# Optimization experiments

Measured on AMD Instinct MI355X. Metric: run time of the kernel, lower is better.

The kernel has to match this reference:

```python
import jax, jax.numpy as jnp
import numpy as np


def setup_inputs() -> dict:
    key = jax.random.key(0)
    kq, kk, kv = jax.random.split(key, 3)
    B, N, D = 8, 4096, 128
    Q = jax.random.normal(kq, (B, N, D), dtype=jnp.float32)
    K = jax.random.normal(kk, (B, N, D), dtype=jnp.float32)
    V = jax.random.normal(kv, (B, N, D), dtype=jnp.float32)
    return {"Q": Q, "K": K, "V": V}


def reference(Q, K, V):
    # attention = Q @ K^T  -> [B, N, N]  (scale=None, mask=None path)
    attention = jnp.einsum('bnd,bmd->bnm', Q, K)
    attention = jax.nn.softmax(attention, axis=-1)
    # context = attention @ V -> [B, N, D]
    context = jnp.einsum('bnm,bmd->bnd', attention, V)
    return context
```

## Files before the change

kernel.cpp:

```cpp
#include <hip/hip_runtime.h>

#define NB 8
#define SEQ 4096
#define DIM 128
#define KVB 64
#define NTILES (SEQ / KVB)
#define HALF 32
#define IMG_BYTES 32768
#define IMG_TOTAL ((size_t)NB * NTILES * IMG_BYTES)
#define PART_ELEMS ((size_t)NB * SEQ * DIM)
#define PART_BYTES (PART_ELEMS * 4)
#define LS_ELEMS ((size_t)NB * SEQ)
#define WS_SPLIT (IMG_TOTAL + 2 * PART_BYTES + 2 * LS_ELEMS * 4)
#define WS_BASIC IMG_TOTAL
#define L2E 1.44269504088896f

typedef _Float16 f16x8 __attribute__((ext_vector_type(8)));
typedef __bf16 bf16x8 __attribute__((ext_vector_type(8)));
typedef float f32x4 __attribute__((ext_vector_type(4)));
typedef float f32x16 __attribute__((ext_vector_type(16)));

struct U4 { unsigned x, y, z, w; };

static __device__ __forceinline__ unsigned cvtpk_bf16(float a, float b) {
  unsigned d;
  asm("v_cvt_pk_bf16_f32 %0, %1, %2" : "=v"(d) : "v"(a), "v"(b));
  return d;
}

#define EXP2(x) __builtin_amdgcn_exp2f(x)

__global__ void prep_kv(const float* __restrict__ K, const float* __restrict__ V,
                        unsigned char* __restrict__ ws) {
  const int t = blockIdx.x;
  const int b = blockIdx.y;
  unsigned char* img = ws + ((size_t)b * NTILES + t) * IMG_BYTES;
  int4* kimg = (int4*)img;
  int4* vimg = (int4*)(img + 16384);
  const float* Kb = K + ((size_t)b * SEQ + t * KVB) * DIM;
  const float* Vb = V + ((size_t)b * SEQ + t * KVB) * DIM;
  const int tid = threadIdx.x;

#pragma unroll
  for (int p = 0; p < 4; ++p) {
    const int un = tid + 256 * p;
    const int kv = un >> 4;
    const int u = (un & 15) ^ (kv & 15);
    const int s = u >> 1, hh = u & 1;
    const float* src = Kb + (size_t)kv * DIM + 16 * s + 8 * hh;
    f16x8 hv;
#pragma unroll
    for (int j = 0; j < 8; ++j) hv[j] = (_Float16)src[j];
    kimg[un] = __builtin_bit_cast(int4, hv);
  }

#pragma unroll
  for (int p = 0; p < 4; ++p) {
    const int un = tid + 256 * p;
    const int rr = un >> 4;
    const int c = (un & 15) ^ (rr & 15);
    const int dhi = c >> 3, slot = c & 7;
    const int s2 = slot >> 1, hh = slot & 1;
    const int d = 64 * dhi + rr;
    bf16x8 hv;
#pragma unroll
    for (int e = 0; e < 8; ++e) {
      const int kv = 16 * s2 + 4 * hh + (e & 3) + 8 * (e >> 2);
      hv[e] = (__bf16)Vb[(size_t)kv * DIM + d];
    }
    vimg[un] = __builtin_bit_cast(int4, hv);
  }
}

__global__ __launch_bounds__(256, 1)
void attn_split(const float* __restrict__ Q, const unsigned char* __restrict__ ws,
                float* __restrict__ part, float* __restrict__ lsw) {
  __shared__ __align__(16) unsigned char smem[65536];

  const int tid = threadIdx.x;
  const int w4 = tid >> 6;
  const int l = tid & 63;
  const int l31 = l & 31;
  const int h = l >> 5;

  const int bid = blockIdx.x;
  const int b = bid & 7;
  const int kvh = (bid >> 3) & 1;
  const int qt = bid >> 4;
  const size_t base = (size_t)b * SEQ * DIM;
  const int qrow0 = qt * 256 + w4 * 64 + l31;

  f16x8 qfA[8], qfB[8];
#pragma unroll
  for (int qb = 0; qb < 2; ++qb) {
    const float* qp = Q + base + (size_t)(qrow0 + 32 * qb) * DIM + 8 * h;
#pragma unroll
    for (int s = 0; s < 8; ++s) {
      f32x4 a = *(const f32x4*)(qp + 16 * s);
      f32x4 c = *(const f32x4*)(qp + 16 * s + 4);
      f16x8 hv;
#pragma unroll
      for (int j = 0; j < 4; ++j) {
        hv[j] = (_Float16)(a[j] * L2E);
        hv[j + 4] = (_Float16)(c[j] * L2E);
      }
      if (qb == 0) qfA[s] = hv; else qfB[s] = hv;
    }
  }

  f32x16 oA[4], oB[4];
#pragma unroll
  for (int j = 0; j < 4; ++j) {
#pragma unroll
    for (int r = 0; r < 16; ++r) { oA[j][r] = 0.f; oB[j][r] = 0.f; }
  }
  float lsA = 0.f, lsB = 0.f;

  const unsigned char* wsb = ws + (size_t)b * NTILES * IMG_BYTES;

  auto STAGE = [&](int t, int bufsel) {
    const unsigned char* src = wsb + (size_t)t * IMG_BYTES + w4 * 8192 + l * 16;
    unsigned char* dst = smem + bufsel * 32768 + w4 * 8192;
#pragma unroll
    for (int i = 0; i < 8; ++i) {
      __builtin_amdgcn_global_load_lds(
          (const __attribute__((address_space(1))) unsigned int*)(src + i * 1024),
          (__attribute__((address_space(3))) unsigned int*)(dst + i * 1024),
          16, 0, 0);
    }
  };

  const int kb2 = (l31 * 256 + ((l31 & 15) * 16)) ^ (h * 16);
  int vb[4];
#pragma unroll
  for (int j = 0; j < 4; ++j) {
    const int rr = 32 * (j & 1) + l31;
    vb[j] = 16384 + rr * 256 + ((((j >> 1) * 8 + h) ^ (rr & 15)) * 16);
  }

  const int t0 = kvh * HALF;
  STAGE(t0, 0);
  __syncthreads();

#pragma unroll 1
  for (int i = 0; i < HALF; ++i) {
    const int cur = i & 1;
    if (i + 1 < HALF) STAGE(t0 + i + 1, cur ^ 1);
    const unsigned char* bufp = smem + cur * 32768;

    f16x8 kk0[8], kk1[8];
#pragma unroll
    for (int s = 0; s < 8; ++s) {
      kk0[s] = *(const f16x8*)(bufp + (kb2 ^ (32 * s)));
      kk1[s] = *(const f16x8*)(bufp + (kb2 ^ (32 * s)) + 8192);
    }

    f32x16 s0, s1, r0, r1;
#pragma unroll
    for (int r = 0; r < 16; ++r) { s0[r] = 0.f; s1[r] = 0.f; r0[r] = 0.f; r1[r] = 0.f; }
    __builtin_amdgcn_s_setprio(1);
#pragma unroll
    for (int s = 0; s < 8; ++s) {
      s0 = __builtin_amdgcn_mfma_f32_32x32x16_f16(kk0[s], qfA[s], s0, 0, 0, 0);
      s1 = __builtin_amdgcn_mfma_f32_32x32x16_f16(kk1[s], qfA[s], s1, 0, 0, 0);
    }
#pragma unroll
    for (int s = 0; s < 8; ++s) {
      r0 = __builtin_amdgcn_mfma_f32_32x32x16_f16(kk0[s], qfB[s], r0, 0, 0, 0);
      r1 = __builtin_amdgcn_mfma_f32_32x32x16_f16(kk1[s], qfB[s], r1, 0, 0, 0);
    }
    __builtin_amdgcn_s_setprio(0);

    bf16x8 vf[16];
#pragma unroll
    for (int s2 = 0; s2 < 4; ++s2) {
#pragma unroll
      for (int j = 0; j < 4; ++j)
        vf[4 * s2 + j] = *(const bf16x8*)(bufp + (vb[j] ^ (32 * s2)));
    }

    float a0 = 0.f, a1 = 0.f, a2 = 0.f, a3 = 0.f;
#pragma unroll
    for (int r = 0; r < 16; r += 4) {
      s0[r + 0] = EXP2(s0[r + 0]); s0[r + 1] = EXP2(s0[r + 1]);
      s0[r + 2] = EXP2(s0[r + 2]); s0[r + 3] = EXP2(s0[r + 3]);
      a0 += s0[r + 0]; a1 += s0[r + 1]; a2 += s0[r + 2]; a3 += s0[r + 3];
    }
#pragma unroll
    for (int r = 0; r < 16; r += 4) {
      s1[r + 0] = EXP2(s1[r + 0]); s1[r + 1] = EXP2(s1[r + 1]);
      s1[r + 2] = EXP2(s1[r + 2]); s1[r + 3] = EXP2(s1[r + 3]);
      a0 += s1[r + 0]; a1 += s1[r + 1]; a2 += s1[r + 2]; a3 += s1[r + 3];
    }
    lsA += (a0 + a1) + (a2 + a3);
    bf16x8 pbA[4];
#pragma unroll
    for (int u = 0; u < 2; ++u) {
      U4 ta = {cvtpk_bf16(s0[8 * u + 0], s0[8 * u + 1]),
               cvtpk_bf16(s0[8 * u + 2], s0[8 * u + 3]),
               cvtpk_bf16(s0[8 * u + 4], s0[8 * u + 5]),
               cvtpk_bf16(s0[8 * u + 6], s0[8 * u + 7])};
      U4 tb = {cvtpk_bf16(s1[8 * u + 0], s1[8 * u + 1]),
               cvtpk_bf16(s1[8 * u + 2], s1[8 * u + 3]),
               cvtpk_bf16(s1[8 * u + 4], s1[8 * u + 5]),
               cvtpk_bf16(s1[8 * u + 6], s1[8 * u + 7])};
      pbA[u] = __builtin_bit_cast(bf16x8, ta);
      pbA[2 + u] = __builtin_bit_cast(bf16x8, tb);
    }

    __builtin_amdgcn_s_setprio(1);
#pragma unroll
    for (int s2 = 0; s2 < 4; ++s2) {
#pragma unroll
      for (int j = 0; j < 4; ++j)
        oA[j] = __builtin_amdgcn_mfma_f32_32x32x16_bf16(vf[4 * s2 + j], pbA[s2],
                                                        oA[j], 0, 0, 0);
    }
    __builtin_amdgcn_s_setprio(0);

    float b0 = 0.f, b1 = 0.f, b2 = 0.f, b3 = 0.f;
#pragma unroll
    for (int r = 0; r < 16; r += 4) {
      r0[r + 0] = EXP2(r0[r + 0]); r0[r + 1] = EXP2(r0[r + 1]);
      r0[r + 2] = EXP2(r0[r + 2]); r0[r + 3] = EXP2(r0[r + 3]);
      b0 += r0[r + 0]; b1 += r0[r + 1]; b2 += r0[r + 2]; b3 += r0[r + 3];
    }
#pragma unroll
    for (int r = 0; r < 16; r += 4) {
      r1[r + 0] = EXP2(r1[r + 0]); r1[r + 1] = EXP2(r1[r + 1]);
      r1[r + 2] = EXP2(r1[r + 2]); r1[r + 3] = EXP2(r1[r + 3]);
      b0 += r1[r + 0]; b1 += r1[r + 1]; b2 += r1[r + 2]; b3 += r1[r + 3];
    }
    lsB += (b0 + b1) + (b2 + b3);
    bf16x8 pbB[4];
#pragma unroll
    for (int u = 0; u < 2; ++u) {
      U4 ta = {cvtpk_bf16(r0[8 * u + 0], r0[8 * u + 1]),
               cvtpk_bf16(r0[8 * u + 2], r0[8 * u + 3]),
               cvtpk_bf16(r0[8 * u + 4], r0[8 * u + 5]),
               cvtpk_bf16(r0[8 * u + 6], r0[8 * u + 7])};
      U4 tb = {cvtpk_bf16(r1[8 * u + 0], r1[8 * u + 1]),
               cvtpk_bf16(r1[8 * u + 2], r1[8 * u + 3]),
               cvtpk_bf16(r1[8 * u + 4], r1[8 * u + 5]),
               cvtpk_bf16(r1[8 * u + 6], r1[8 * u + 7])};
      pbB[u] = __builtin_bit_cast(bf16x8, ta);
      pbB[2 + u] = __builtin_bit_cast(bf16x8, tb);
    }

    __builtin_amdgcn_s_setprio(1);
#pragma unroll
    for (int s2 = 0; s2 < 4; ++s2) {
#pragma unroll
      for (int j = 0; j < 4; ++j)
        oB[j] = __builtin_amdgcn_mfma_f32_32x32x16_bf16(vf[4 * s2 + j], pbB[s2],
                                                        oB[j], 0, 0, 0);
    }
    __builtin_amdgcn_s_setprio(0);
    __syncthreads();
  }

  lsA += __shfl_xor(lsA, 32);
  lsB += __shfl_xor(lsB, 32);
  float* P = part + (size_t)kvh * PART_ELEMS + base;
#pragma unroll
  for (int qb = 0; qb < 2; ++qb) {
    float* Pb = P + (size_t)(qrow0 + 32 * qb) * DIM;
#pragma unroll
    for (int j = 0; j < 4; ++j) {
#pragma unroll
      for (int rq = 0; rq < 4; ++rq) {
        f32x4 res;
#pragma unroll
        for (int r = 0; r < 4; ++r)
          res[r] = qb == 0 ? oA[j][4 * rq + r] : oB[j][4 * rq + r];
        *(f32x4*)(Pb + 32 * j + 8 * rq + 4 * h) = res;
      }
    }
  }
  if (h == 0) {
    lsw[(size_t)kvh * LS_ELEMS + b * SEQ + qrow0] = lsA;
    lsw[(size_t)kvh * LS_ELEMS + b * SEQ + qrow0 + 32] = lsB;
  }
}

__global__ void combine(const float* __restrict__ part,
                        const float* __restrict__ lsw,
                        float* __restrict__ out) {
  const size_t idx = (size_t)blockIdx.x * 256 + threadIdx.x;
  const f32x4 a = ((const f32x4*)part)[idx];
  const f32x4 b = ((const f32x4*)(part + PART_ELEMS))[idx];
  const size_t row = idx >> 5;
  const float inv = 1.0f / (lsw[row] + lsw[LS_ELEMS + row]);
  f32x4 r;
#pragma unroll
  for (int j = 0; j < 4; ++j) r[j] = (a[j] + b[j]) * inv;
  ((f32x4*)out)[idx] = r;
}

__global__ __launch_bounds__(256, 2)
void attn_fwd15(const float* __restrict__ Q, const unsigned char* __restrict__ ws,
                float* __restrict__ O) {
  __shared__ __align__(16) unsigned char smem[65536];

  const int tid = threadIdx.x;
  const int w4 = tid >> 6;
  const int l = tid & 63;
  const int l31 = l & 31;
  const int h = l >> 5;

  const int bid = blockIdx.x;
  const int b = bid & 7;
  const int qt = bid >> 3;
  const size_t base = (size_t)b * SEQ * DIM;
  const int qrow = qt * 128 + w4 * 32 + l31;

  f16x8 qf[8];
  {
    const float* qp = Q + base + (size_t)qrow * DIM + 8 * h;
#pragma unroll
    for (int s = 0; s < 8; ++s) {
      f32x4 a = *(const f32x4*)(qp + 16 * s);
      f32x4 c = *(const f32x4*)(qp + 16 * s + 4);
      f16x8 hv;
#pragma unroll
      for (int j = 0; j < 4; ++j) {
        hv[j] = (_Float16)(a[j] * L2E);
        hv[j + 4] = (_Float16)(c[j] * L2E);
      }
      qf[s] = hv;
    }
  }

  f32x16 o[4];
#pragma unroll
  for (int j = 0; j < 4; ++j) {
#pragma unroll
    for (int r = 0; r < 16; ++r) o[j][r] = 0.f;
  }
  float ls = 0.f;

  const unsigned char* wsb = ws + (size_t)b * NTILES * IMG_BYTES;

  auto STAGE = [&](int t, int bufsel) {
    const unsigned char* src = wsb + (size_t)t * IMG_BYTES + w4 * 8192 + l * 16;
    unsigned char* dst = smem + bufsel * 32768 + w4 * 8192;
#pragma unroll
    for (int i = 0; i < 8; ++i) {
      __builtin_amdgcn_global_load_lds(
          (const __attribute__((address_space(1))) unsigned int*)(src + i * 1024),
          (__attribute__((address_space(3))) unsigned int*)(dst + i * 1024),
          16, 0, 0);
    }
  };

  const int kb2 = (l31 * 256 + ((l31 & 15) * 16)) ^ (h * 16);
  int vb[4];
#pragma unroll
  for (int j = 0; j < 4; ++j) {
    const int rr = 32 * (j & 1) + l31;
    vb[j] = 16384 + rr * 256 + ((((j >> 1) * 8 + h) ^ (rr & 15)) * 16);
  }

  STAGE(0, 0);
  __syncthreads();

  for (int t = 0; t < NTILES; ++t) {
    const int cur = t & 1;
    if (t + 1 < NTILES) STAGE(t + 1, cur ^ 1);
    const unsigned char* bufp = smem + cur * 32768;

    f32x16 s0, s1;
#pragma unroll
    for (int r = 0; r < 16; ++r) { s0[r] = 0.f; s1[r] = 0.f; }
    __builtin_amdgcn_s_setprio(1);
#pragma unroll
    for (int s = 0; s < 8; ++s) {
      f16x8 k0 = *(const f16x8*)(bufp + (kb2 ^ (32 * s)));
      s0 = __builtin_amdgcn_mfma_f32_32x32x16_f16(k0, qf[s], s0, 0, 0, 0);
    }
#pragma unroll
    for (int s = 0; s < 8; ++s) {
      f16x8 k1 = *(const f16x8*)(bufp + (kb2 ^ (32 * s)) + 8192);
      s1 = __builtin_amdgcn_mfma_f32_32x32x16_f16(k1, qf[s], s1, 0, 0, 0);
    }
    __builtin_amdgcn_s_setprio(0);

    float a0 = 0.f, a1 = 0.f, a2 = 0.f, a3 = 0.f;
#pragma unroll
    for (int r = 0; r < 16; r += 4) {
      s0[r + 0] = EXP2(s0[r + 0]); s0[r + 1] = EXP2(s0[r + 1]);
      s0[r + 2] = EXP2(s0[r + 2]); s0[r + 3] = EXP2(s0[r + 3]);
      a0 += s0[r + 0]; a1 += s0[r + 1]; a2 += s0[r + 2]; a3 += s0[r + 3];
    }
    bf16x8 pb0[2];
#pragma unroll
    for (int u = 0; u < 2; ++u) {
      U4 t0 = {cvtpk_bf16(s0[8 * u + 0], s0[8 * u + 1]),
               cvtpk_bf16(s0[8 * u + 2], s0[8 * u + 3]),
               cvtpk_bf16(s0[8 * u + 4], s0[8 * u + 5]),
               cvtpk_bf16(s0[8 * u + 6], s0[8 * u + 7])};
      pb0[u] = __builtin_bit_cast(bf16x8, t0);
    }

    __builtin_amdgcn_s_setprio(1);
#pragma unroll
    for (int s2 = 0; s2 < 2; ++s2) {
#pragma unroll
      for (int j = 0; j < 4; ++j) {
        bf16x8 vf = *(const bf16x8*)(bufp + (vb[j] ^ (32 * s2)));
        o[j] = __builtin_amdgcn_mfma_f32_32x32x16_bf16(vf, pb0[s2], o[j], 0, 0, 0);
      }
    }
    __builtin_amdgcn_s_setprio(0);

#pragma unroll
    for (int r = 0; r < 16; r += 4) {
      s1[r + 0] = EXP2(s1[r + 0]); s1[r + 1] = EXP2(s1[r + 1]);
      s1[r + 2] = EXP2(s1[r + 2]); s1[r + 3] = EXP2(s1[r + 3]);
      a0 += s1[r + 0]; a1 += s1[r + 1]; a2 += s1[r + 2]; a3 += s1[r + 3];
    }
    ls += (a0 + a1) + (a2 + a3);
    bf16x8 pb1[2];
#pragma unroll
    for (int u = 0; u < 2; ++u) {
      U4 t1 = {cvtpk_bf16(s1[8 * u + 0], s1[8 * u + 1]),
               cvtpk_bf16(s1[8 * u + 2], s1[8 * u + 3]),
               cvtpk_bf16(s1[8 * u + 4], s1[8 * u + 5]),
               cvtpk_bf16(s1[8 * u + 6], s1[8 * u + 7])};
      pb1[u] = __builtin_bit_cast(bf16x8, t1);
    }

    __builtin_amdgcn_s_setprio(1);
#pragma unroll
    for (int s2 = 2; s2 < 4; ++s2) {
#pragma unroll
      for (int j = 0; j < 4; ++j) {
        bf16x8 vf = *(const bf16x8*)(bufp + (vb[j] ^ (32 * s2)));
        o[j] = __builtin_amdgcn_mfma_f32_32x32x16_bf16(vf, pb1[s2 - 2], o[j], 0, 0, 0);
      }
    }
    __builtin_amdgcn_s_setprio(0);
    __syncthreads();
  }

  ls += __shfl_xor(ls, 32);
  const float inv = 1.0f / ls;
  float* Ob = O + base + (size_t)qrow * DIM;
#pragma unroll
  for (int j = 0; j < 4; ++j) {
#pragma unroll
    for (int rq = 0; rq < 4; ++rq) {
      f32x4 res;
#pragma unroll
      for (int r = 0; r < 4; ++r) res[r] = o[j][4 * rq + r] * inv;
      *(f32x4*)(Ob + 32 * j + 8 * rq + 4 * h) = res;
    }
  }
}

extern "C" void kernel_launch(void* const* d_in, const int* in_sizes, int n_in,
                              void* d_out, int out_size, void* d_ws,
                              size_t ws_size, hipStream_t stream) {
  const float* Q = (const float*)d_in[0];
  const float* K = (const float*)d_in[1];
  const float* V = (const float*)d_in[2];
  float* Out = (float*)d_out;
  unsigned char* ws = (unsigned char*)d_ws;
  if (ws_size < WS_BASIC) return;
  prep_kv<<<dim3(NTILES, NB), dim3(256), 0, stream>>>(K, V, ws);
  if (ws_size >= WS_SPLIT) {
    float* part = (float*)(ws + IMG_TOTAL);
    float* lsw = (float*)(ws + IMG_TOTAL + 2 * PART_BYTES);
    attn_split<<<dim3(256), dim3(256), 0, stream>>>(Q, ws, part, lsw);
    combine<<<dim3(PART_ELEMS / 4 / 256), dim3(256), 0, stream>>>(part, lsw, Out);
  } else {
    attn_fwd15<<<dim3(SEQ / 128 * NB), dim3(256), 0, stream>>>(Q, ws, Out);
  }
}
```

Baseline: 103.3 us.

## Halve per-wave query rows in split kernel to run two blocks per CU

Each wave of the split-KV attention kernel now handles 32 query rows instead of 64. The grid doubles to 512 blocks and launch bounds allow 2 blocks per CU. K and V fragments are loaded from LDS just before each MFMA instead of being preloaded into registers, and the PV product for the first half-tile is interleaved before the second exp pass. The aim is lower register pressure and more resident waves to hide latency, at the cost of reading K/V from LDS twice as often per query row. The 64KB shared buffer per block may limit how many blocks actually fit per CU.

```diff
diff --git a/kernel.cpp b/kernel.cpp
--- a/kernel.cpp
+++ b/kernel.cpp
@@ -72,7 +72,7 @@
   }
 }
 
-__global__ __launch_bounds__(256, 1)
+__global__ __launch_bounds__(256, 2)
 void attn_split(const float* __restrict__ Q, const unsigned char* __restrict__ ws,
                 float* __restrict__ part, float* __restrict__ lsw) {
   __shared__ __align__(16) unsigned char smem[65536];
@@ -88,12 +88,11 @@
   const int kvh = (bid >> 3) & 1;
   const int qt = bid >> 4;
   const size_t base = (size_t)b * SEQ * DIM;
-  const int qrow0 = qt * 256 + w4 * 64 + l31;
-
-  f16x8 qfA[8], qfB[8];
-#pragma unroll
-  for (int qb = 0; qb < 2; ++qb) {
-    const float* qp = Q + base + (size_t)(qrow0 + 32 * qb) * DIM + 8 * h;
+  const int qrow = qt * 128 + w4 * 32 + l31;
+
+  f16x8 qf[8];
+  {
+    const float* qp = Q + base + (size_t)qrow * DIM + 8 * h;
 #pragma unroll
     for (int s = 0; s < 8; ++s) {
       f32x4 a = *(const f32x4*)(qp + 16 * s);
@@ -104,17 +103,17 @@
         hv[j] = (_Float16)(a[j] * L2E);
         hv[j + 4] = (_Float16)(c[j] * L2E);
       }
-      if (qb == 0) qfA[s] = hv; else qfB[s] = hv;
-    }
-  }
-
-  f32x16 oA[4], oB[4];
-#pragma unroll
-  for (int j = 0; j < 4; ++j) {
-#pragma unroll
-    for (int r = 0; r < 16; ++r) { oA[j][r] = 0.f; oB[j][r] = 0.f; }
-  }
-  float lsA = 0.f, lsB = 0.f;
+      qf[s] = hv;
+    }
+  }
+
+  f32x16 o[4];
+#pragma unroll
+  for (int j = 0; j < 4; ++j) {
+#pragma unroll
+    for (int r = 0; r < 16; ++r) o[j][r] = 0.f;
+  }
+  float ls = 0.f;
 
   const unsigned char* wsb = ws + (size_t)b * NTILES * IMG_BYTES;
 
@@ -148,36 +147,21 @@
     if (i + 1 < HALF) STAGE(t0 + i + 1, cur ^ 1);
     const unsigned char* bufp = smem + cur * 32768;
 
-    f16x8 kk0[8], kk1[8];
-#pragma unroll
-    for (int s = 0; s < 8; ++s) {
-      kk0[s] = *(const f16x8*)(bufp + (kb2 ^ (32 * s)));
-      kk1[s] = *(const f16x8*)(bufp + (kb2 ^ (32 * s)) + 8192);
-    }
-
-    f32x16 s0, s1, r0, r1;
-#pragma unroll
-    for (int r = 0; r < 16; ++r) { s0[r] = 0.f; s1[r] = 0.f; r0[r] = 0.f; r1[r] = 0.f; }
-    __builtin_amdgcn_s_setprio(1);
-#pragma unroll
-    for (int s = 0; s < 8; ++s) {
-      s0 = __builtin_amdgcn_mfma_f32_32x32x16_f16(kk0[s], qfA[s], s0, 0, 0, 0);
-      s1 = __builtin_amdgcn_mfma_f32_32x32x16_f16(kk1[s], qfA[s], s1, 0, 0, 0);
-    }
-#pragma unroll
-    for (int s = 0; s < 8; ++s) {
-      r0 = __builtin_amdgcn_mfma_f32_32x32x16_f16(kk0[s], qfB[s], r0, 0, 0, 0);
-      r1 = __builtin_amdgcn_mfma_f32_32x32x16_f16(kk1[s], qfB[s], r1, 0, 0, 0);
-    }
-    __builtin_amdgcn_s_setprio(0);
-
-    bf16x8 vf[16];
-#pragma unroll
-    for (int s2 = 0; s2 < 4; ++s2) {
-#pragma unroll
-      for (int j = 0; j < 4; ++j)
-        vf[4 * s2 + j] = *(const bf16x8*)(bufp + (vb[j] ^ (32 * s2)));
-    }
+    f32x16 s0, s1;
+#pragma unroll
+    for (int r = 0; r < 16; ++r) { s0[r] = 0.f; s1[r] = 0.f; }
+    __builtin_amdgcn_s_setprio(1);
+#pragma unroll
+    for (int s = 0; s < 8; ++s) {
+      f16x8 k0 = *(const f16x8*)(bufp + (kb2 ^ (32 * s)));
+      s0 = __builtin_amdgcn_mfma_f32_32x32x16_f16(k0, qf[s], s0, 0, 0, 0);
+    }
+#pragma unroll
+    for (int s = 0; s < 8; ++s) {
+      f16x8 k1 = *(const f16x8*)(bufp + (kb2 ^ (32 * s)) + 8192);
+      s1 = __builtin_amdgcn_mfma_f32_32x32x16_f16(k1, qf[s], s1, 0, 0, 0);
+    }
+    __builtin_amdgcn_s_setprio(0);
 
     float a0 = 0.f, a1 = 0.f, a2 = 0.f, a3 = 0.f;
 #pragma unroll
@@ -186,101 +170,70 @@
       s0[r + 2] = EXP2(s0[r + 2]); s0[r + 3] = EXP2(s0[r + 3]);
       a0 += s0[r + 0]; a1 += s0[r + 1]; a2 += s0[r + 2]; a3 += s0[r + 3];
     }
+    bf16x8 pb0[2];
+#pragma unroll
+    for (int u = 0; u < 2; ++u) {
+      U4 t0v = {cvtpk_bf16(s0[8 * u + 0], s0[8 * u + 1]),
+                cvtpk_bf16(s0[8 * u + 2], s0[8 * u + 3]),
+                cvtpk_bf16(s0[8 * u + 4], s0[8 * u + 5]),
+                cvtpk_bf16(s0[8 * u + 6], s0[8 * u + 7])};
+      pb0[u] = __builtin_bit_cast(bf16x8, t0v);
+    }
+
+    __builtin_amdgcn_s_setprio(1);
+#pragma unroll
+    for (int s2 = 0; s2 < 2; ++s2) {
+#pragma unroll
+      for (int j = 0; j < 4; ++j) {
+        bf16x8 vf = *(const bf16x8*)(bufp + (vb[j] ^ (32 * s2)));
+        o[j] = __builtin_amdgcn_mfma_f32_32x32x16_bf16(vf, pb0[s2], o[j], 0, 0, 0);
+      }
+    }
+    __builtin_amdgcn_s_setprio(0);
+
 #pragma unroll
     for (int r = 0; r < 16; r += 4) {
       s1[r + 0] = EXP2(s1[r + 0]); s1[r + 1] = EXP2(s1[r + 1]);
       s1[r + 2] = EXP2(s1[r + 2]); s1[r + 3] = EXP2(s1[r + 3]);
       a0 += s1[r + 0]; a1 += s1[r + 1]; a2 += s1[r + 2]; a3 += s1[r + 3];
     }
-    lsA += (a0 + a1) + (a2 + a3);
-    bf16x8 pbA[4];
+    ls += (a0 + a1) + (a2 + a3);
+    bf16x8 pb1[2];
 #pragma unroll
     for (int u = 0; u < 2; ++u) {
-      U4 ta = {cvtpk_bf16(s0[8 * u + 0], s0[8 * u + 1]),
-               cvtpk_bf16(s0[8 * u + 2], s0[8 * u + 3]),
-               cvtpk_bf16(s0[8 * u + 4], s0[8 * u + 5]),
-               cvtpk_bf16(s0[8 * u + 6], s0[8 * u + 7])};
-      U4 tb = {cvtpk_bf16(s1[8 * u + 0], s1[8 * u + 1]),
-               cvtpk_bf16(s1[8 * u + 2], s1[8 * u + 3]),
-               cvtpk_bf16(s1[8 * u + 4], s1[8 * u + 5]),
-               cvtpk_bf16(s1[8 * u + 6], s1[8 * u + 7])};
-      pbA[u] = __builtin_bit_cast(bf16x8, ta);
-      pbA[2 + u] = __builtin_bit_cast(bf16x8, tb);
-    }
-
-    __builtin_amdgcn_s_setprio(1);
-#pragma unroll
-    for (int s2 = 0; s2 < 4; ++s2) {
-#pragma unroll
-      for (int j = 0; j < 4; ++j)
-        oA[j] = __builtin_amdgcn_mfma_f32_32x32x16_bf16(vf[4 * s2 + j], pbA[s2],
-                                                        oA[j], 0, 0, 0);
-    }
-    __builtin_amdgcn_s_setprio(0);
-
-    float b0 = 0.f, b1 = 0.f, b2 = 0.f, b3 = 0.f;
-#pragma unroll
-    for (int r = 0; r < 16; r += 4) {
-      r0[r + 0] = EXP2(r0[r + 0]); r0[r + 1] = EXP2(r0[r + 1]);
-      r0[r + 2] = EXP2(r0[r + 2]); r0[r + 3] = EXP2(r0[r + 3]);
-      b0 += r0[r + 0]; b1 += r0[r + 1]; b2 += r0[r + 2]; b3 += r0[r + 3];
-    }
-#pragma unroll
-    for (int r = 0; r < 16; r += 4) {
-      r1[r + 0] = EXP2(r1[r + 0]); r1[r + 1] = EXP2(r1[r + 1]);
-      r1[r + 2] = EXP2(r1[r + 2]); r1[r + 3] = EXP2(r1[r + 3]);
-      b0 += r1[r + 0]; b1 += r1[r + 1]; b2 += r1[r + 2]; b3 += r1[r + 3];
-    }
-    lsB += (b0 + b1) + (b2 + b3);
-    bf16x8 pbB[4];
-#pragma unroll
-    for (int u = 0; u < 2; ++u) {
-      U4 ta = {cvtpk_bf16(r0[8 * u + 0], r0[8 * u + 1]),
-               cvtpk_bf16(r0[8 * u + 2], r0[8 * u + 3]),
-               cvtpk_bf16(r0[8 * u + 4], r0[8 * u + 5]),
-               cvtpk_bf16(r0[8 * u + 6], r0[8 * u + 7])};
-      U4 tb = {cvtpk_bf16(r1[8 * u + 0], r1[8 * u + 1]),
-               cvtpk_bf16(r1[8 * u + 2], r1[8 * u + 3]),
-               cvtpk_bf16(r1[8 * u + 4], r1[8 * u + 5]),
-               cvtpk_bf16(r1[8 * u + 6], r1[8 * u + 7])};
-      pbB[u] = __builtin_bit_cast(bf16x8, ta);
-      pbB[2 + u] = __builtin_bit_cast(bf16x8, tb);
-    }
-
-    __builtin_amdgcn_s_setprio(1);
-#pragma unroll
-    for (int s2 = 0; s2 < 4; ++s2) {
-#pragma unroll
-      for (int j = 0; j < 4; ++j)
-        oB[j] = __builtin_amdgcn_mfma_f32_32x32x16_bf16(vf[4 * s2 + j], pbB[s2],
-                                                        oB[j], 0, 0, 0);
+      U4 t1v = {cvtpk_bf16(s1[8 * u + 0], s1[8 * u + 1]),
+                cvtpk_bf16(s1[8 * u + 2], s1[8 * u + 3]),
+                cvtpk_bf16(s1[8 * u + 4], s1[8 * u + 5]),
+                cvtpk_bf16(s1[8 * u + 6], s1[8 * u + 7])};
+      pb1[u] = __builtin_bit_cast(bf16x8, t1v);
+    }
+
+    __builtin_amdgcn_s_setprio(1);
+#pragma unroll
+    for (int s2 = 2; s2 < 4; ++s2) {
+#pragma unroll
+      for (int j = 0; j < 4; ++j) {
+        bf16x8 vf = *(const bf16x8*)(bufp + (vb[j] ^ (32 * s2)));
+        o[j] = __builtin_amdgcn_mfma_f32_32x32x16_bf16(vf, pb1[s2 - 2], o[j], 0, 0, 0);
+      }
     }
     __builtin_amdgcn_s_setprio(0);
     __syncthreads();
   }
 
-  lsA += __shfl_xor(lsA, 32);
-  lsB += __shfl_xor(lsB, 32);
-  float* P = part + (size_t)kvh * PART_ELEMS + base;
-#pragma unroll
-  for (int qb = 0; qb < 2; ++qb) {
-    float* Pb = P + (size_t)(qrow0 + 32 * qb) * DIM;
-#pragma unroll
-    for (int j = 0; j < 4; ++j) {
-#pragma unroll
-      for (int rq = 0; rq < 4; ++rq) {
-        f32x4 res;
-#pragma unroll
-        for (int r = 0; r < 4; ++r)
-          res[r] = qb == 0 ? oA[j][4 * rq + r] : oB[j][4 * rq + r];
-        *(f32x4*)(Pb + 32 * j + 8 * rq + 4 * h) = res;
-      }
-    }
-  }
-  if (h == 0) {
-    lsw[(size_t)kvh * LS_ELEMS + b * SEQ + qrow0] = lsA;
-    lsw[(size_t)kvh * LS_ELEMS + b * SEQ + qrow0 + 32] = lsB;
-  }
+  ls += __shfl_xor(ls, 32);
+  float* Pb = part + (size_t)kvh * PART_ELEMS + base + (size_t)qrow * DIM;
+#pragma unroll
+  for (int j = 0; j < 4; ++j) {
+#pragma unroll
+    for (int rq = 0; rq < 4; ++rq) {
+      f32x4 res;
+#pragma unroll
+      for (int r = 0; r < 4; ++r) res[r] = o[j][4 * rq + r];
+      *(f32x4*)(Pb + 32 * j + 8 * rq + 4 * h) = res;
+    }
+  }
+  if (h == 0) lsw[(size_t)kvh * LS_ELEMS + b * SEQ + qrow] = ls;
 }
 
 __global__ void combine(const float* __restrict__ part,
@@ -471,7 +424,7 @@
   if (ws_size >= WS_SPLIT) {
     float* part = (float*)(ws + IMG_TOTAL);
     float* lsw = (float*)(ws + IMG_TOTAL + 2 * PART_BYTES);
-    attn_split<<<dim3(256), dim3(256), 0, stream>>>(Q, ws, part, lsw);
+    attn_split<<<dim3(512), dim3(256), 0, stream>>>(Q, ws, part, lsw);
     combine<<<dim3(PART_ELEMS / 4 / 256), dim3(256), 0, stream>>>(part, lsw, Out);
   } else {
     attn_fwd15<<<dim3(SEQ / 128 * NB), dim3(256), 0, stream>>>(Q, ws, Out);
```

New measurement: 101.8 us. Within noise of the previous version (-1.4%).
